# Kernel optimization log

Hardware: AMD Instinct MI355X
Metric: run time of the kernel (lower is better)

The kernel has to match this reference:

```python
import jax, jax.numpy as jnp
import numpy as np

B, T, U = 4, 256, 100
H_ENC, H_DEC = 512, 512
INPUT_SIZE = H_ENC + H_DEC  # 1024, joint='concat'
INNER = 512
VOCAB = 1024


def setup_inputs() -> dict:
    key = jax.random.key(0)
    k1, k2, k3, k4, k5, k6 = jax.random.split(key, 6)
    s_in = 1.0 / np.sqrt(INPUT_SIZE)
    s_h = 1.0 / np.sqrt(INNER)
    return {
        "enc_state": jax.random.normal(k1, (B, T, H_ENC), dtype=jnp.float32),
        "dec_state": jax.random.normal(k2, (B, U, H_DEC), dtype=jnp.float32),
        # mlp[0]: Linear(input_size -> inner): W1 [inner, input_size], b1 [inner]
        "W1": jax.random.uniform(k3, (INNER, INPUT_SIZE), jnp.float32, -s_in, s_in),
        "b1": jax.random.uniform(k4, (INNER,), jnp.float32, -s_in, s_in),
        # mlp[2]: Linear(inner -> vocab): W2 [vocab, inner], b2 [vocab]
        "W2": jax.random.uniform(k5, (VOCAB, INNER), jnp.float32, -s_h, s_h),
        "b2": jax.random.uniform(k6, (VOCAB,), jnp.float32, -s_h, s_h),
    }


def reference(enc_state, dec_state, W1, b1, W2, b2):
    # joint='concat': concat([enc broadcast over U, dec broadcast over T], -1)
    # then Linear -> tanh -> Linear.
    # Mathematically identical fused form: split W1 into enc/dec column blocks,
    # project each at native size, broadcast-add.
    h_enc = H_ENC
    W1e = W1[:, :h_enc]   # [inner, H_enc]
    W1d = W1[:, h_enc:]   # [inner, H_dec]
    pe = jnp.einsum('bth,ih->bti', enc_state, W1e)  # [B,T,inner]
    pd = jnp.einsum('buh,ih->bui', dec_state, W1d)  # [B,U,inner]
    hidden = jnp.tanh(pe[:, :, None, :] + pd[:, None, :, :] + b1)  # [B,T,U,inner]
    joint = jnp.einsum('btui,vi->btuv', hidden, W2) + b2  # [B,T,U,vocab]
    return joint
```

## Files before the change

kernel.cpp:

```cpp
#include <hip/hip_runtime.h>
#include <hip/hip_bf16.h>

#define NB 4
#define NT 256
#define NU 100
#define NH 512
#define NI 512
#define NV 1024
#define MROWS (NB * NT * NU)

typedef __attribute__((ext_vector_type(4))) float f32x4;
typedef __attribute__((ext_vector_type(8))) __bf16 bf16x8;

static __device__ __forceinline__ unsigned int f2bf(float f) {
  unsigned int u = __float_as_uint(f);
  return (u + 0x7FFFu + ((u >> 16) & 1u)) >> 16;
}

static __device__ __forceinline__ float fast_tanh(float x) {
  float e = __expf(2.f * x);
  return 1.f - 2.f * __builtin_amdgcn_rcpf(1.f + e);
}

static __device__ __forceinline__ unsigned int cvt_pk_bf16(float lo, float hi) {
  unsigned int r;
  asm("v_cvt_pk_bf16_f32 %0, %1, %2" : "=v"(r) : "v"(lo), "v"(hi));
  return r;
}

__global__ __launch_bounds__(256) void prep_kernel(
    const float* __restrict__ enc, const float* __restrict__ dec,
    const float* __restrict__ W1, const float* __restrict__ W2,
    float* __restrict__ pe, float* __restrict__ pd,
    unsigned short* __restrict__ w2f) {
  const int bx = blockIdx.x;
  const int tx = threadIdx.x;
  if (bx >= 23) {
    int c = ((bx - 23) * 8 + blockIdx.y) * 256 + tx;
    int lr = c & 15, lq = (c >> 4) & 3;
    int cb = (c >> 6) & 15, kt = (c >> 10) & 15, nt = (c >> 14) & 3;
    int v = nt * 256 + cb * 16 + lr;
    int k = kt * 32 + lq * 8;
    const float* src = W2 + (size_t)v * NI + k;
    float4 a = *(const float4*)src;
    float4 b = *(const float4*)(src + 4);
    uint4 o;
    o.x = f2bf(a.x) | (f2bf(a.y) << 16);
    o.y = f2bf(a.z) | (f2bf(a.w) << 16);
    o.z = f2bf(b.x) | (f2bf(b.y) << 16);
    o.w = f2bf(b.z) | (f2bf(b.w) << 16);
    *(uint4*)(w2f + (size_t)c * 8) = o;
    return;
  }
  __shared__ float As[64][17];
  __shared__ float Bs[64][17];
  const float* A;
  float* P;
  int Mrows, colOff, row0;
  if (bx < 16) { A = enc; P = pe; Mrows = NB * NT; colOff = 0;  row0 = bx * 64; }
  else         { A = dec; P = pd; Mrows = NB * NU; colOff = NH; row0 = (bx - 16) * 64; }
  const int col0 = blockIdx.y * 64;
  const int tr = tx >> 4, tc = tx & 15;
  const int lr = tx >> 2, lc = (tx & 3) * 4;
  float acc[4][4] = {};
  for (int k0 = 0; k0 < NH; k0 += 16) {
    float4 av = make_float4(0.f, 0.f, 0.f, 0.f);
    if (row0 + lr < Mrows)
      av = *(const float4*)(A + (size_t)(row0 + lr) * NH + k0 + lc);
    float4 bv = *(const float4*)(W1 + (size_t)(col0 + lr) * (NH + NH) + colOff + k0 + lc);
    As[lr][lc] = av.x; As[lr][lc + 1] = av.y; As[lr][lc + 2] = av.z; As[lr][lc + 3] = av.w;
    Bs[lr][lc] = bv.x; Bs[lr][lc + 1] = bv.y; Bs[lr][lc + 2] = bv.z; Bs[lr][lc + 3] = bv.w;
    __syncthreads();
#pragma unroll
    for (int kk = 0; kk < 16; ++kk) {
      float a4[4], b4[4];
#pragma unroll
      for (int i = 0; i < 4; ++i) { a4[i] = As[tr * 4 + i][kk]; b4[i] = Bs[tc * 4 + i][kk]; }
#pragma unroll
      for (int i = 0; i < 4; ++i)
#pragma unroll
        for (int j = 0; j < 4; ++j) acc[i][j] = fmaf(a4[i], b4[j], acc[i][j]);
    }
    __syncthreads();
  }
#pragma unroll
  for (int i = 0; i < 4; ++i) {
    int r = row0 + tr * 4 + i;
    if (r < Mrows) {
#pragma unroll
      for (int j = 0; j < 4; ++j)
        P[(size_t)r * NI + col0 + tc * 4 + j] = acc[i][j];
    }
  }
}

__global__ __launch_bounds__(512, 2) void fused_joint_kernel(
    const float* __restrict__ pe, const float* __restrict__ pd,
    const float* __restrict__ b1, const unsigned short* __restrict__ w2f,
    const float* __restrict__ b2, float* __restrict__ out) {
  __shared__ unsigned char ldsA[131072];
  const int tx = threadIdx.x;
  const int R0 = blockIdx.x * 128;
  const int lane = tx & 63, wid = tx >> 6;
  const int wr = wid >> 2, wc = wid & 3;
  const int lr = lane & 15, lq = lane >> 4;

  const unsigned short* w2base = w2f + ((size_t)(wc * 4) * 64 + lq * 16 + lr) * 8;
#define LOADB(DST, G) do {                                                    \
    const unsigned short* s_ = w2base + ((size_t)(G) << 13);                  \
    DST##0 = *(const bf16x8*)(s_);                                            \
    DST##1 = *(const bf16x8*)(s_ + 512);                                      \
    DST##2 = *(const bf16x8*)(s_ + 1024);                                     \
    DST##3 = *(const bf16x8*)(s_ + 1536);                                     \
  } while (0)

  bf16x8 bA0, bA1, bA2, bA3, bB0, bB1, bB2, bB3;
  LOADB(bA, 0);

#pragma unroll 2
  for (int pass = 0; pass < 16; ++pass) {
    int idx = pass * 512 + tx;
    int row = idx >> 6;
    int g8 = idx & 63;
    int i0 = g8 * 8;
    int grow = R0 + row;
    int b = grow / (NT * NU);
    int rem = grow - b * (NT * NU);
    int t = rem / NU;
    int u = rem - t * NU;
    const float* peP = pe + (size_t)(b * NT + t) * NI + i0;
    const float* pdP = pd + (size_t)(b * NU + u) * NI + i0;
    float4 p0 = *(const float4*)peP, p1 = *(const float4*)(peP + 4);
    float4 q0 = *(const float4*)pdP, q1 = *(const float4*)(pdP + 4);
    float4 c0 = *(const float4*)(b1 + i0), c1 = *(const float4*)(b1 + i0 + 4);
    uint4 pk;
    pk.x = cvt_pk_bf16(fast_tanh(p0.x + q0.x + c0.x), fast_tanh(p0.y + q0.y + c0.y));
    pk.y = cvt_pk_bf16(fast_tanh(p0.z + q0.z + c0.z), fast_tanh(p0.w + q0.w + c0.w));
    pk.z = cvt_pk_bf16(fast_tanh(p1.x + q1.x + c1.x), fast_tanh(p1.y + q1.y + c1.y));
    pk.w = cvt_pk_bf16(fast_tanh(p1.z + q1.z + c1.z), fast_tanh(p1.w + q1.w + c1.w));
    *(uint4*)(ldsA + row * 1024 + ((g8 ^ (row & 7)) << 4)) = pk;
  }
  __syncthreads();

  f32x4 acc[4][4];
#pragma unroll
  for (int mf = 0; mf < 4; ++mf)
#pragma unroll
    for (int nf = 0; nf < 4; ++nf)
#pragma unroll
      for (int z = 0; z < 4; ++z) acc[mf][nf][z] = 0.f;

#define COMPUTE(BV, G) do {                                                   \
    const int kt_ = (G) & 15;                                                 \
    bf16x8 af_[4];                                                            \
    _Pragma("unroll")                                                         \
    for (int mf = 0; mf < 4; ++mf) {                                          \
      int row_ = wr * 64 + mf * 16 + lr;                                      \
      af_[mf] = *(const bf16x8*)(ldsA + row_ * 1024 +                         \
                                 (((kt_ * 4 + lq) ^ (lr & 7)) << 4));         \
    }                                                                         \
    __builtin_amdgcn_s_setprio(1);                                            \
    _Pragma("unroll")                                                         \
    for (int mf = 0; mf < 4; ++mf) {                                          \
      acc[mf][0] = __builtin_amdgcn_mfma_f32_16x16x32_bf16(af_[mf], BV##0, acc[mf][0], 0, 0, 0); \
      acc[mf][1] = __builtin_amdgcn_mfma_f32_16x16x32_bf16(af_[mf], BV##1, acc[mf][1], 0, 0, 0); \
      acc[mf][2] = __builtin_amdgcn_mfma_f32_16x16x32_bf16(af_[mf], BV##2, acc[mf][2], 0, 0, 0); \
      acc[mf][3] = __builtin_amdgcn_mfma_f32_16x16x32_bf16(af_[mf], BV##3, acc[mf][3], 0, 0, 0); \
    }                                                                         \
    __builtin_amdgcn_s_setprio(0);                                            \
    if (kt_ == 15) {                                                          \
      const int np_ = (G) >> 4;                                               \
      _Pragma("unroll")                                                       \
      for (int nf = 0; nf < 4; ++nf) {                                        \
        int col_ = np_ * 256 + wc * 64 + nf * 16 + lr;                        \
        float bb_ = b2[col_];                                                 \
        _Pragma("unroll")                                                     \
        for (int mf = 0; mf < 4; ++mf) {                                      \
          _Pragma("unroll")                                                   \
          for (int j = 0; j < 4; ++j) {                                       \
            int grow_ = R0 + wr * 64 + mf * 16 + lq * 4 + j;                  \
            out[(size_t)grow_ * NV + col_] = acc[mf][nf][j] + bb_;            \
            acc[mf][nf][j] = 0.f;                                             \
          }                                                                   \
        }                                                                     \
      }                                                                       \
    }                                                                         \
  } while (0)

  for (int g = 0; g < 64; g += 2) {
    LOADB(bB, g + 1);
    COMPUTE(bA, g);
    if (g + 2 < 64) LOADB(bA, g + 2);
    COMPUTE(bB, g + 1);
  }
#undef COMPUTE
#undef LOADB
}

extern "C" void kernel_launch(void* const* d_in, const int* in_sizes, int n_in,
                              void* d_out, int out_size, void* d_ws, size_t ws_size,
                              hipStream_t stream) {
  const float* enc = (const float*)d_in[0];
  const float* dec = (const float*)d_in[1];
  const float* W1  = (const float*)d_in[2];
  const float* b1  = (const float*)d_in[3];
  const float* W2  = (const float*)d_in[4];
  const float* b2  = (const float*)d_in[5];
  float* out = (float*)d_out;
  char* ws = (char*)d_ws;

  float* pe = (float*)ws;
  float* pd = (float*)(ws + (2u << 20));
  unsigned short* w2f = (unsigned short*)(ws + (3u << 20));

  prep_kernel<<<dim3(55, 8), 256, 0, stream>>>(enc, dec, W1, W2, pe, pd, w2f);
  fused_joint_kernel<<<MROWS / 128, 512, 0, stream>>>(pe, pd, b1, w2f, b2, out);
}
```

Before: 243.9 us.

## Halve row tile to 64 rows per block and software-pipeline LDS A-fragment loads

```diff
diff --git a/kernel.cpp b/kernel.cpp
--- a/kernel.cpp
+++ b/kernel.cpp
@@ -94,13 +94,13 @@
   }
 }
 
-__global__ __launch_bounds__(512, 2) void fused_joint_kernel(
+__global__ __launch_bounds__(512, 4) void fused_joint_kernel(
     const float* __restrict__ pe, const float* __restrict__ pd,
     const float* __restrict__ b1, const unsigned short* __restrict__ w2f,
     const float* __restrict__ b2, float* __restrict__ out) {
-  __shared__ unsigned char ldsA[131072];
+  __shared__ unsigned char ldsA[65536];
   const int tx = threadIdx.x;
-  const int R0 = blockIdx.x * 128;
+  const int R0 = blockIdx.x * 64;
   const int lane = tx & 63, wid = tx >> 6;
   const int wr = wid >> 2, wc = wid & 3;
   const int lr = lane & 15, lq = lane >> 4;
@@ -118,7 +118,7 @@
   LOADB(bA, 0);
 
 #pragma unroll 2
-  for (int pass = 0; pass < 16; ++pass) {
+  for (int pass = 0; pass < 8; ++pass) {
     int idx = pass * 512 + tx;
     int row = idx >> 6;
     int g8 = idx & 63;
@@ -142,43 +142,46 @@
   }
   __syncthreads();
 
-  f32x4 acc[4][4];
-#pragma unroll
-  for (int mf = 0; mf < 4; ++mf)
+  f32x4 acc[2][4];
+#pragma unroll
+  for (int mf = 0; mf < 2; ++mf)
 #pragma unroll
     for (int nf = 0; nf < 4; ++nf)
 #pragma unroll
       for (int z = 0; z < 4; ++z) acc[mf][nf][z] = 0.f;
 
-#define COMPUTE(BV, G) do {                                                   \
-    const int kt_ = (G) & 15;                                                 \
-    bf16x8 af_[4];                                                            \
-    _Pragma("unroll")                                                         \
-    for (int mf = 0; mf < 4; ++mf) {                                          \
-      int row_ = wr * 64 + mf * 16 + lr;                                      \
-      af_[mf] = *(const bf16x8*)(ldsA + row_ * 1024 +                         \
-                                 (((kt_ * 4 + lq) ^ (lr & 7)) << 4));         \
-    }                                                                         \
+  const int aOff0 = (wr * 32 + lr) * 1024;
+  const int aOff1 = (wr * 32 + 16 + lr) * 1024;
+  const int rx = lr & 7;
+
+#define LOADA(AF, G) do {                                                     \
+    const int so_ = ((((G) & 15) * 4 + lq) ^ rx) << 4;                        \
+    AF##0 = *(const bf16x8*)(ldsA + aOff0 + so_);                             \
+    AF##1 = *(const bf16x8*)(ldsA + aOff1 + so_);                             \
+  } while (0)
+
+#define MFMA8(AF, BV, G) do {                                                 \
     __builtin_amdgcn_s_setprio(1);                                            \
-    _Pragma("unroll")                                                         \
-    for (int mf = 0; mf < 4; ++mf) {                                          \
-      acc[mf][0] = __builtin_amdgcn_mfma_f32_16x16x32_bf16(af_[mf], BV##0, acc[mf][0], 0, 0, 0); \
-      acc[mf][1] = __builtin_amdgcn_mfma_f32_16x16x32_bf16(af_[mf], BV##1, acc[mf][1], 0, 0, 0); \
-      acc[mf][2] = __builtin_amdgcn_mfma_f32_16x16x32_bf16(af_[mf], BV##2, acc[mf][2], 0, 0, 0); \
-      acc[mf][3] = __builtin_amdgcn_mfma_f32_16x16x32_bf16(af_[mf], BV##3, acc[mf][3], 0, 0, 0); \
-    }                                                                         \
+    acc[0][0] = __builtin_amdgcn_mfma_f32_16x16x32_bf16(AF##0, BV##0, acc[0][0], 0, 0, 0); \
+    acc[0][1] = __builtin_amdgcn_mfma_f32_16x16x32_bf16(AF##0, BV##1, acc[0][1], 0, 0, 0); \
+    acc[0][2] = __builtin_amdgcn_mfma_f32_16x16x32_bf16(AF##0, BV##2, acc[0][2], 0, 0, 0); \
+    acc[0][3] = __builtin_amdgcn_mfma_f32_16x16x32_bf16(AF##0, BV##3, acc[0][3], 0, 0, 0); \
+    acc[1][0] = __builtin_amdgcn_mfma_f32_16x16x32_bf16(AF##1, BV##0, acc[1][0], 0, 0, 0); \
+    acc[1][1] = __builtin_amdgcn_mfma_f32_16x16x32_bf16(AF##1, BV##1, acc[1][1], 0, 0, 0); \
+    acc[1][2] = __builtin_amdgcn_mfma_f32_16x16x32_bf16(AF##1, BV##2, acc[1][2], 0, 0, 0); \
+    acc[1][3] = __builtin_amdgcn_mfma_f32_16x16x32_bf16(AF##1, BV##3, acc[1][3], 0, 0, 0); \
     __builtin_amdgcn_s_setprio(0);                                            \
-    if (kt_ == 15) {                                                          \
+    if (((G) & 15) == 15) {                                                   \
       const int np_ = (G) >> 4;                                               \
       _Pragma("unroll")                                                       \
       for (int nf = 0; nf < 4; ++nf) {                                        \
         int col_ = np_ * 256 + wc * 64 + nf * 16 + lr;                        \
         float bb_ = b2[col_];                                                 \
         _Pragma("unroll")                                                     \
-        for (int mf = 0; mf < 4; ++mf) {                                      \
+        for (int mf = 0; mf < 2; ++mf) {                                      \
           _Pragma("unroll")                                                   \
           for (int j = 0; j < 4; ++j) {                                       \
-            int grow_ = R0 + wr * 64 + mf * 16 + lq * 4 + j;                  \
+            int grow_ = R0 + wr * 32 + mf * 16 + lq * 4 + j;                  \
             out[(size_t)grow_ * NV + col_] = acc[mf][nf][j] + bb_;            \
             acc[mf][nf][j] = 0.f;                                             \
           }                                                                   \
@@ -187,13 +190,21 @@
     }                                                                         \
   } while (0)
 
+  bf16x8 aC0, aC1, aN0, aN1;
+  LOADA(aC, 0);
+
   for (int g = 0; g < 64; g += 2) {
     LOADB(bB, g + 1);
-    COMPUTE(bA, g);
-    if (g + 2 < 64) LOADB(bA, g + 2);
-    COMPUTE(bB, g + 1);
-  }
-#undef COMPUTE
+    LOADA(aN, g + 1);
+    MFMA8(aC, bA, g);
+    if (g + 2 < 64) {
+      LOADB(bA, g + 2);
+      LOADA(aC, g + 2);
+    }
+    MFMA8(aN, bB, g + 1);
+  }
+#undef MFMA8
+#undef LOADA
 #undef LOADB
 }
 
@@ -214,5 +225,5 @@
   unsigned short* w2f = (unsigned short*)(ws + (3u << 20));
 
   prep_kernel<<<dim3(55, 8), 256, 0, stream>>>(enc, dec, W1, W2, pe, pd, w2f);
-  fused_joint_kernel<<<MROWS / 128, 512, 0, stream>>>(pe, pd, b1, w2f, b2, out);
-}
+  fused_joint_kernel<<<MROWS / 64, 512, 0, stream>>>(pe, pd, b1, w2f, b2, out);
+}
```

Measured after the change: 239.4 us. Within noise of the previous version (-1.9%).

## Split joint GEMM into 64-row by 512-column blocks for higher occupancy

Applied to the files above, without the earlier changes.

```diff
diff --git a/kernel.cpp b/kernel.cpp
--- a/kernel.cpp
+++ b/kernel.cpp
@@ -94,20 +94,22 @@
   }
 }
 
-__global__ __launch_bounds__(512, 2) void fused_joint_kernel(
+__global__ __launch_bounds__(512, 4) void fused_joint_kernel(
     const float* __restrict__ pe, const float* __restrict__ pd,
     const float* __restrict__ b1, const unsigned short* __restrict__ w2f,
     const float* __restrict__ b2, float* __restrict__ out) {
-  __shared__ unsigned char ldsA[131072];
+  __shared__ unsigned char ldsA[65536];
   const int tx = threadIdx.x;
-  const int R0 = blockIdx.x * 128;
+  const int R0 = (blockIdx.x >> 1) * 64;
+  const int nh = blockIdx.x & 1;
   const int lane = tx & 63, wid = tx >> 6;
-  const int wr = wid >> 2, wc = wid & 3;
   const int lr = lane & 15, lq = lane >> 4;
 
-  const unsigned short* w2base = w2f + ((size_t)(wc * 4) * 64 + lq * 16 + lr) * 8;
-#define LOADB(DST, G) do {                                                    \
-    const unsigned short* s_ = w2base + ((size_t)(G) << 13);                  \
+  const unsigned short* w2base =
+      w2f + ((size_t)(nh * 2 + (wid >> 2)) * 16384 +
+             (size_t)((wid & 3) * 4) * 64 + lq * 16 + lr) * 8;
+#define LOADB(DST, KT) do {                                                   \
+    const unsigned short* s_ = w2base + ((size_t)(KT) << 13);                 \
     DST##0 = *(const bf16x8*)(s_);                                            \
     DST##1 = *(const bf16x8*)(s_ + 512);                                      \
     DST##2 = *(const bf16x8*)(s_ + 1024);                                     \
@@ -118,7 +120,7 @@
   LOADB(bA, 0);
 
 #pragma unroll 2
-  for (int pass = 0; pass < 16; ++pass) {
+  for (int pass = 0; pass < 8; ++pass) {
     int idx = pass * 512 + tx;
     int row = idx >> 6;
     int g8 = idx & 63;
@@ -150,15 +152,14 @@
 #pragma unroll
       for (int z = 0; z < 4; ++z) acc[mf][nf][z] = 0.f;
 
-#define COMPUTE(BV, G) do {                                                   \
-    const int kt_ = (G) & 15;                                                 \
+  const int rx = lr & 7;
+
+#define COMPUTE(BV, KT) do {                                                  \
     bf16x8 af_[4];                                                            \
+    const int so_ = (((KT) * 4 + lq) ^ rx) << 4;                              \
     _Pragma("unroll")                                                         \
-    for (int mf = 0; mf < 4; ++mf) {                                          \
-      int row_ = wr * 64 + mf * 16 + lr;                                      \
-      af_[mf] = *(const bf16x8*)(ldsA + row_ * 1024 +                         \
-                                 (((kt_ * 4 + lq) ^ (lr & 7)) << 4));         \
-    }                                                                         \
+    for (int mf = 0; mf < 4; ++mf)                                            \
+      af_[mf] = *(const bf16x8*)(ldsA + (mf * 16 + lr) * 1024 + so_);         \
     __builtin_amdgcn_s_setprio(1);                                            \
     _Pragma("unroll")                                                         \
     for (int mf = 0; mf < 4; ++mf) {                                          \
@@ -168,33 +169,30 @@
       acc[mf][3] = __builtin_amdgcn_mfma_f32_16x16x32_bf16(af_[mf], BV##3, acc[mf][3], 0, 0, 0); \
     }                                                                         \
     __builtin_amdgcn_s_setprio(0);                                            \
-    if (kt_ == 15) {                                                          \
-      const int np_ = (G) >> 4;                                               \
-      _Pragma("unroll")                                                       \
-      for (int nf = 0; nf < 4; ++nf) {                                        \
-        int col_ = np_ * 256 + wc * 64 + nf * 16 + lr;                        \
-        float bb_ = b2[col_];                                                 \
-        _Pragma("unroll")                                                     \
-        for (int mf = 0; mf < 4; ++mf) {                                      \
-          _Pragma("unroll")                                                   \
-          for (int j = 0; j < 4; ++j) {                                       \
-            int grow_ = R0 + wr * 64 + mf * 16 + lq * 4 + j;                  \
-            out[(size_t)grow_ * NV + col_] = acc[mf][nf][j] + bb_;            \
-            acc[mf][nf][j] = 0.f;                                             \
-          }                                                                   \
-        }                                                                     \
-      }                                                                       \
-    }                                                                         \
   } while (0)
 
-  for (int g = 0; g < 64; g += 2) {
-    LOADB(bB, g + 1);
-    COMPUTE(bA, g);
-    if (g + 2 < 64) LOADB(bA, g + 2);
-    COMPUTE(bB, g + 1);
+  for (int kt = 0; kt < 16; kt += 2) {
+    LOADB(bB, kt + 1);
+    COMPUTE(bA, kt);
+    if (kt + 2 < 16) LOADB(bA, kt + 2);
+    COMPUTE(bB, kt + 1);
   }
 #undef COMPUTE
 #undef LOADB
+
+#pragma unroll
+  for (int nf = 0; nf < 4; ++nf) {
+    int col = nh * 512 + wid * 64 + nf * 16 + lr;
+    float bb = b2[col];
+#pragma unroll
+    for (int mf = 0; mf < 4; ++mf) {
+#pragma unroll
+      for (int j = 0; j < 4; ++j) {
+        int grow = R0 + mf * 16 + lq * 4 + j;
+        out[(size_t)grow * NV + col] = acc[mf][nf][j] + bb;
+      }
+    }
+  }
 }
 
 extern "C" void kernel_launch(void* const* d_in, const int* in_sizes, int n_in,
@@ -214,5 +212,5 @@
   unsigned short* w2f = (unsigned short*)(ws + (3u << 20));
 
   prep_kernel<<<dim3(55, 8), 256, 0, stream>>>(enc, dec, W1, W2, pe, pd, w2f);
-  fused_joint_kernel<<<MROWS / 128, 512, 0, stream>>>(pe, pd, b1, w2f, b2, out);
-}
+  fused_joint_kernel<<<(MROWS / 64) * 2, 512, 0, stream>>>(pe, pd, b1, w2f, b2, out);
+}
```

New measurement: 258.2 us. 5.8% more time.
